# Kernel optimization log

Measured on AMD Instinct MI355X. Metric: run time of the kernel, lower is better.

The kernel has to match this reference:

```python
import jax, jax.numpy as jnp
import numpy as np

N, V, F, H, B, HID = 256, 32, 128, 8, 8, 64
R_MAX = 5.0
DH = F // H


def fc_edges(n):
    a = np.arange(n)
    s, r = np.meshgrid(a, a, indexing="ij")
    m = s != r
    return jnp.asarray(s[m]), jnp.asarray(r[m])

SENDERS, RECEIVERS = fc_edges(N)
E = N * (N - 1)


def sph_harmonics(u):
    # u: [..., 3] unit vectors -> [..., 15] = l=1(3)+l=2(5)+l=3(7), e3nn 'component' normalization
    x, y, z = u[..., 0], u[..., 1], u[..., 2]
    s3 = 3.0 ** 0.5; s5 = 5.0 ** 0.5; s7 = 7.0 ** 0.5
    s15 = 15.0 ** 0.5; s105 = 105.0 ** 0.5
    s35_8 = (35.0 / 8.0) ** 0.5; s21_8 = (21.0 / 8.0) ** 0.5
    l1 = [s3 * y, s3 * z, s3 * x]
    l2 = [s15 * x * y, s15 * y * z, 0.5 * s5 * (3 * z * z - 1),
          s15 * x * z, 0.5 * s15 * (x * x - y * y)]
    l3 = [s35_8 * y * (3 * x * x - y * y), s105 * x * y * z,
          s21_8 * y * (5 * z * z - 1), 0.5 * s7 * z * (5 * z * z - 3),
          s21_8 * x * (5 * z * z - 1), 0.5 * s105 * z * (x * x - y * y),
          s35_8 * x * (x * x - 3 * y * y)]
    return jnp.stack(l1 + l2 + l3, axis=-1)


def radial_embed(lengths):
    # Bessel basis (e3nn.bessel) times soft envelope (e3nn.soft_envelope)
    x = jnp.maximum(lengths, 1e-6)[..., None]
    k = jnp.arange(1, B + 1, dtype=lengths.dtype)
    bes = (2.0 / R_MAX) ** 0.5 * jnp.sin(k * jnp.pi * x / R_MAX) / x
    def sus(t):
        return jnp.where(t > 0, jnp.exp(-1.0 / jnp.where(t > 0, t, 1.0)), 0.0)
    env = 1.2 * sus(2.0 * (1.0 - lengths / R_MAX)) / sus(jnp.asarray(2.0))
    return bes * env[..., None]


def setup_inputs():
    key = jax.random.key(0)
    ks = jax.random.split(key, 16)
    def w(k, shape):
        return jax.random.normal(k, shape, jnp.float32) / (shape[0] ** 0.5)
    D_edge = 2 * F + V * B
    return {
        "positions": jax.random.normal(ks[0], (N, V, 3), jnp.float32),
        "features": jax.random.normal(ks[1], (N, F), jnp.float32),
        "We1": w(ks[2], (D_edge, HID)), "be1": jnp.zeros((HID,), jnp.float32),
        "We2": w(ks[3], (HID, HID)), "be2": jnp.zeros((HID,), jnp.float32),
        "W_q": w(ks[4], (F, F)), "W_k": w(ks[5], (HID, F)),
        "W_v": w(ks[6], (F, F)), "W_vec": w(ks[7], (HID, V)),
        "W_mix": w(ks[8], (V, V)),
        "M1": w(ks[9], (F, HID)), "bm1": jnp.zeros((HID,), jnp.float32),
        "M2": w(ks[10], (HID, HID)), "bm2": jnp.zeros((HID,), jnp.float32),
        "M3": w(ks[11], (HID, F)), "bm3": jnp.zeros((F,), jnp.float32),
    }


def reference(positions, features, We1, be1, We2, be2, W_q, W_k, W_v, W_vec,
              W_mix, M1, bm1, M2, bm2, M3, bm3):
    act = jax.nn.selu
    s, r = SENDERS, RECEIVERS
    vectors = positions[s] - positions[r]                        # [E, V, 3]
    lengths = jnp.sqrt(jnp.sum(vectors * vectors, -1) + 1e-18)   # [E, V] safe_norm
    unit = vectors / lengths[..., None]
    sph = sph_harmonics(unit)                                    # [E, V, 15]
    radial = radial_embed(lengths).reshape(E, V * B)             # [E, V*B]
    edge_weight_cutoff = jnp.ones((E,), positions.dtype)

    # edge MLP on invariants (radial embedding + src/dst scalar features)
    edge_in = jnp.concatenate([features[s], features[r], radial], -1)
    h = act(edge_in @ We1 + be1)
    h = act(h @ We2 + be2)                                       # [E, HID]

    # multi-head attention over incoming edges per node (segment softmax)
    q = (features @ W_q).reshape(N, H, DH)
    k = (h @ W_k).reshape(E, H, DH)
    logit = jnp.einsum("ehd,ehd->eh", k, q[r]) / (DH ** 0.5)
    lmax = jax.ops.segment_max(logit, r, num_segments=N)
    ex = edge_weight_cutoff[:, None] * jnp.exp(logit - lmax[r])
    denom = jax.ops.segment_sum(ex, r, num_segments=N)
    alpha = ex / (denom[r] + 1e-12)                              # [E, H]

    # invariant (0e) values
    v = (features[s] @ W_v).reshape(E, H, DH)
    inv_agg = jax.ops.segment_sum(alpha[..., None] * v, r, num_segments=N).reshape(N, F)

    # equivariant (1o) values: scalar-gated l=1 spherical harmonics (sqrt(3)*unit)
    coeff = h @ W_vec                                            # [E, V]
    alpha_v = jnp.repeat(alpha, V // H, axis=1)                  # [E, V]
    vec_msg = ((alpha_v * coeff) * (3.0 ** 0.5))[..., None] * unit  # [E, V, 3]
    vec_agg = jax.ops.segment_sum(vec_msg, r, num_segments=N)    # [N, V, 3]
    vec_out = jnp.einsum("nvc,vw->nwc", vec_agg, W_mix)

    # final invariant MLP + residuals
    hi = act(inv_agg @ M1 + bm1)
    hi = act(hi @ M2 + bm2)
    inv_out = hi @ M3 + bm3
    return (vec_out + positions, inv_out + features)
```

## Files before the change

kernel.cpp:

```cpp
#include <hip/hip_runtime.h>
#include <hip/hip_bf16.h>

#define NN 256
#define VC 32
#define FD 128

typedef unsigned int uint32;
typedef unsigned short u16;
typedef __attribute__((ext_vector_type(8))) short bf16x8;
typedef __attribute__((ext_vector_type(4))) float f32x4;

__device__ __forceinline__ float selu_f(float x) {
    const float lam = 1.0507009873554805f;
    const float la  = 1.7580993408473766f;
    return x > 0.f ? lam * x : la * (__expf(x) - 1.f);
}

__device__ __forceinline__ u16 f32_to_bf16_rne(float f) {
    uint32 u = __float_as_uint(f);
    uint32 r = (u + 0x7fffu + ((u >> 16) & 1u)) >> 16;
    return (u16)r;
}

__device__ __forceinline__ float bf16_to_f32(u16 h) {
    return __uint_as_float(((uint32)h) << 16);
}

__global__ __launch_bounds__(256) void k1_pre(
    const float* __restrict__ feat, const float* __restrict__ We1,
    const float* __restrict__ be1, const float* __restrict__ Wq,
    const float* __restrict__ Wk, const float* __restrict__ Wv,
    const float* __restrict__ Wvec, const float* __restrict__ We2,
    const float* __restrict__ pos,
    float* __restrict__ A, float* __restrict__ Bf, u16* __restrict__ kqb,
    u16* __restrict__ w1b, u16* __restrict__ we2b, u16* __restrict__ wvb,
    u16* __restrict__ fvtH, u16* __restrict__ fvtL,
    u16* __restrict__ ptH, u16* __restrict__ ptL,
    float* __restrict__ lgg2, u16* __restrict__ cfg2)
{
    __shared__ float fl[FD];
    __shared__ float ql[FD];
    const int n = blockIdx.x;
    const int t = threadIdx.x;
    {
        const int gid = n*256 + t;
        if (gid < 16384) {
            const int c = gid >> 8, k = gid & 255;
            w1b[gid] = f32_to_bf16_rne(We1[(256 + k)*64 + c]);
        } else if (gid < 20480) {
            const int o = gid - 16384;
            const int c = o >> 6, k = o & 63;
            we2b[o] = f32_to_bf16_rne(We2[k*64 + c]);
        } else if (gid < 22528) {
            const int o = gid - 20480;
            const int v = o >> 6, k = o & 63;
            wvb[o] = f32_to_bf16_rne(Wvec[k*32 + v]);
        }
    }
    if (t < FD) fl[t] = feat[n*FD + t];
    __syncthreads();
    if (t < 64) {
        float a = 0.f;
        for (int i = 0; i < FD; ++i) a = fmaf(fl[i], We1[i*64 + t], a);
        A[n*64 + t] = a;
    } else if (t < 128) {
        const int j = t - 64;
        float a = be1[j];
        for (int i = 0; i < FD; ++i) a = fmaf(fl[i], We1[(FD+i)*64 + j], a);
        Bf[n*64 + j] = a;
    } else {
        const int j = t - 128;
        float a = 0.f;
        for (int i = 0; i < FD; ++i) a = fmaf(fl[i], Wq[i*FD + j], a);
        ql[j] = a * 0.25f;
    }
    if (t < FD) {
        float a = 0.f;
        for (int i = 0; i < FD; ++i) a = fmaf(fl[i], Wv[i*FD + t], a);
        const u16 hi = f32_to_bf16_rne(a);
        const u16 lo = f32_to_bf16_rne(a - bf16_to_f32(hi));
        fvtH[t*256 + n] = hi;
        fvtL[t*256 + n] = lo;
    }
    if (t < 128) {
        const int v = t >> 2, c = t & 3;
        const float val = (c < 3) ? pos[(n*VC + v)*3 + c] : 1.0f;
        const u16 hi = f32_to_bf16_rne(val);
        const u16 lo = f32_to_bf16_rne(val - bf16_to_f32(hi));
        ptH[(v*4+c)*256 + n] = hi;
        ptL[(v*4+c)*256 + n] = lo;
    }
    if (t < 8)  lgg2[n*2048 + t*256 + n] = -1e30f;
    if (t < 32) cfg2[n*8192 + t*256 + n] = 0;
    __syncthreads();
    for (int o = t; o < 512; o += 256) {
        const int h = o >> 6, j = o & 63;
        float a = 0.f;
        #pragma unroll
        for (int d = 0; d < 16; ++d)
            a = fmaf(Wk[j*FD + h*16 + d], ql[h*16 + d], a);
        kqb[n*512 + o] = f32_to_bf16_rne(a);
    }
}

__global__ __launch_bounds__(256) void k2_edge(
    const float* __restrict__ pos, const float* __restrict__ be2,
    const float* __restrict__ Ag, const float* __restrict__ Bfg,
    const u16* __restrict__ w1b, const u16* __restrict__ we2b,
    const u16* __restrict__ wvb, const u16* __restrict__ kqb,
    float* __restrict__ lgg2, u16* __restrict__ cfg2)
{
    __shared__ u16 rad[8192];
    __shared__ u16 h1b[32*64];
    __shared__ u16 h2b[32*64];
    __shared__ float invl[32*33];

    const int t = threadIdx.x;
    const int wave = t >> 6, l = t & 63;
    const int li = l & 15, q = l >> 4;
    const int mh = wave >> 1, eh = wave & 1;
    const int r = blockIdx.x >> 2, part = blockIdx.x & 3;
    const int e = eh*16 + li;
    const int swz16 = (e & 7) << 3;

    bf16x8 w1A[2][8];
    #pragma unroll
    for (int mt = 0; mt < 2; ++mt) {
        const int c = mh*32 + mt*16 + li;
        #pragma unroll
        for (int kb = 0; kb < 8; ++kb)
            w1A[mt][kb] = *(const bf16x8*)(w1b + c*256 + kb*32 + q*8);
    }
    bf16x8 we2A[2][2];
    #pragma unroll
    for (int mt = 0; mt < 2; ++mt) {
        const int c2 = mh*32 + mt*16 + li;
        #pragma unroll
        for (int kb = 0; kb < 2; ++kb)
            we2A[mt][kb] = *(const bf16x8*)(we2b + c2*64 + kb*32 + q*8);
    }
    bf16x8 wvA[2];
    {
        const int v = mh*16 + li;
        #pragma unroll
        for (int kb = 0; kb < 2; ++kb)
            wvA[kb] = *(const bf16x8*)(wvb + v*64 + kb*32 + q*8);
    }
    bf16x8 kqA[2];
    if (li < 8) {
        #pragma unroll
        for (int kb = 0; kb < 2; ++kb)
            kqA[kb] = *(const bf16x8*)(kqb + r*512 + li*64 + kb*32 + q*8);
    } else {
        #pragma unroll
        for (int kb = 0; kb < 2; ++kb)
            #pragma unroll
            for (int j = 0; j < 8; ++j) kqA[kb][j] = 0;
    }
    float bfreg[2][4], be2reg[2][4];
    #pragma unroll
    for (int mt = 0; mt < 2; ++mt)
        #pragma unroll
        for (int rg = 0; rg < 4; ++rg) {
            const int c = mh*32 + mt*16 + q*4 + rg;
            bfreg[mt][rg] = Bfg[r*64 + c];
            be2reg[mt][rg] = be2[c];
        }

    for (int it = 0; it < 2; ++it) {
        const int s0 = (part*2 + it) * 32;
        const int sp = s0 + e;
        int s = sp + (sp >= r ? 1 : 0); if (s > 255) s = 255;
        __syncthreads();

        float As[2][4];
        #pragma unroll
        for (int mt = 0; mt < 2; ++mt)
            #pragma unroll
            for (int rg = 0; rg < 4; ++rg)
                As[mt][rg] = Ag[s*64 + mh*32 + mt*16 + q*4 + rg];

        {
            const int ep = t & 31, vg = t >> 5;
            const int spp = s0 + ep;
            int sv = spp + (spp >= r ? 1 : 0); if (sv > 255) sv = 255;
            #pragma unroll
            for (int kk = 0; kk < 4; ++kk) {
                const int v = vg*4 + kk;
                const float* ps = pos + (sv*VC + v)*3;
                const float* pr = pos + (r*VC + v)*3;
                const float dx = ps[0]-pr[0], dy = ps[1]-pr[1], dz = ps[2]-pr[2];
                const float d2 = fmaf(dx,dx,fmaf(dy,dy,dz*dz)) + 1e-18f;
                const float len = sqrtf(d2);
                invl[ep*33 + v] = rsqrtf(d2);
                const float x = fmaxf(len, 1e-6f);
                const float tt2 = 2.f - 0.4f*len;
                const float env = tt2 > 0.f ? 1.9784655248401538f * __expf(-1.f/tt2) : 0.f;
                const float coefc = 0.6324555320336759f * env / x;
                float s_cur, c1;
                __sincosf(0.6283185307179586f * x, &s_cur, &c1);
                const float c2x = 2.f * c1;
                float s_prev = 0.f;
                union { uint4 u4; u16 us[8]; } pk;
                #pragma unroll
                for (int b = 0; b < 8; ++b) {
                    pk.us[b] = f32_to_bf16_rne(coefc * s_cur);
                    const float s_next = fmaf(c2x, s_cur, -s_prev);
                    s_prev = s_cur; s_cur = s_next;
                }
                *(uint4*)((char*)rad + ((ep*512 + v*16) ^ ((ep & 15) << 4))) = pk.u4;
            }
        }
        __syncthreads();

        f32x4 d1[2] = {{0.f,0.f,0.f,0.f},{0.f,0.f,0.f,0.f}};
        #pragma unroll
        for (int kb = 0; kb < 8; ++kb) {
            const bf16x8 rf = *(const bf16x8*)((const char*)rad +
                                ((e*512 + (kb*4+q)*16) ^ ((e & 15) << 4)));
            d1[0] = __builtin_amdgcn_mfma_f32_16x16x32_bf16(w1A[0][kb], rf, d1[0], 0, 0, 0);
            d1[1] = __builtin_amdgcn_mfma_f32_16x16x32_bf16(w1A[1][kb], rf, d1[1], 0, 0, 0);
        }
        #pragma unroll
        for (int mt = 0; mt < 2; ++mt) {
            const int c0 = mh*32 + mt*16 + q*4;
            const u16 p0 = f32_to_bf16_rne(selu_f(d1[mt][0] + As[mt][0] + bfreg[mt][0]));
            const u16 p1 = f32_to_bf16_rne(selu_f(d1[mt][1] + As[mt][1] + bfreg[mt][1]));
            const u16 p2 = f32_to_bf16_rne(selu_f(d1[mt][2] + As[mt][2] + bfreg[mt][2]));
            const u16 p3 = f32_to_bf16_rne(selu_f(d1[mt][3] + As[mt][3] + bfreg[mt][3]));
            *(uint32*)&h1b[e*64 + ((c0)     ^ swz16)] = (uint32)p0 | ((uint32)p1 << 16);
            *(uint32*)&h1b[e*64 + ((c0 + 2) ^ swz16)] = (uint32)p2 | ((uint32)p3 << 16);
        }
        __syncthreads();

        f32x4 d2[2] = {{0.f,0.f,0.f,0.f},{0.f,0.f,0.f,0.f}};
        #pragma unroll
        for (int kb = 0; kb < 2; ++kb) {
            const bf16x8 hb = *(const bf16x8*)&h1b[e*64 + ((kb*32 + q*8) ^ swz16)];
            d2[0] = __builtin_amdgcn_mfma_f32_16x16x32_bf16(we2A[0][kb], hb, d2[0], 0, 0, 0);
            d2[1] = __builtin_amdgcn_mfma_f32_16x16x32_bf16(we2A[1][kb], hb, d2[1], 0, 0, 0);
        }
        #pragma unroll
        for (int mt = 0; mt < 2; ++mt) {
            const int c0 = mh*32 + mt*16 + q*4;
            const u16 p0 = f32_to_bf16_rne(selu_f(d2[mt][0] + be2reg[mt][0]));
            const u16 p1 = f32_to_bf16_rne(selu_f(d2[mt][1] + be2reg[mt][1]));
            const u16 p2 = f32_to_bf16_rne(selu_f(d2[mt][2] + be2reg[mt][2]));
            const u16 p3 = f32_to_bf16_rne(selu_f(d2[mt][3] + be2reg[mt][3]));
            *(uint32*)&h2b[e*64 + ((c0)     ^ swz16)] = (uint32)p0 | ((uint32)p1 << 16);
            *(uint32*)&h2b[e*64 + ((c0 + 2) ^ swz16)] = (uint32)p2 | ((uint32)p3 << 16);
        }
        __syncthreads();

        f32x4 d3 = {0.f,0.f,0.f,0.f};
        f32x4 dl = {0.f,0.f,0.f,0.f};
        #pragma unroll
        for (int kb = 0; kb < 2; ++kb) {
            const bf16x8 hb = *(const bf16x8*)&h2b[e*64 + ((kb*32 + q*8) ^ swz16)];
            d3 = __builtin_amdgcn_mfma_f32_16x16x32_bf16(wvA[kb], hb, d3, 0, 0, 0);
            if (mh == 0)
                dl = __builtin_amdgcn_mfma_f32_16x16x32_bf16(kqA[kb], hb, dl, 0, 0, 0);
        }
        if (sp < 255) {
            #pragma unroll
            for (int rg = 0; rg < 4; ++rg) {
                const int v = mh*16 + q*4 + rg;
                cfg2[(size_t)r*8192 + v*256 + s] =
                    f32_to_bf16_rne(d3[rg] * 1.7320508075688772f * invl[e*33 + v]);
            }
            if (mh == 0 && q < 2) {
                #pragma unroll
                for (int rg = 0; rg < 4; ++rg)
                    lgg2[(size_t)r*2048 + (q*4+rg)*256 + s] = dl[rg];
            }
        }
    }
}

__global__ __launch_bounds__(64) void k3b_agg(
    const float* __restrict__ lgg2, const u16* __restrict__ cfg2,
    const u16* __restrict__ fvtH, const u16* __restrict__ fvtL,
    const u16* __restrict__ ptH, const u16* __restrict__ ptL,
    float* __restrict__ inv, float* __restrict__ vec4)
{
    const int l = threadIdx.x, li = l & 15, q = l >> 4;
    const int b = blockIdx.x;
    if (b < 128) {
        const int h = b >> 4, r0 = (b & 15) * 16;
        bf16x8 fH[8], fL[8];
        #pragma unroll
        for (int kb = 0; kb < 8; ++kb) {
            fH[kb] = *(const bf16x8*)(fvtH + (h*16+li)*256 + kb*32 + q*8);
            fL[kb] = *(const bf16x8*)(fvtL + (h*16+li)*256 + kb*32 + q*8);
        }
        const float* lgr = lgg2 + (size_t)(r0+li)*2048 + h*256;
        float mx = -3.0e38f;
        #pragma unroll
        for (int kb = 0; kb < 8; ++kb) {
            const float4 g0 = *(const float4*)(lgr + kb*32 + q*8);
            const float4 g1 = *(const float4*)(lgr + kb*32 + q*8 + 4);
            mx = fmaxf(mx, fmaxf(fmaxf(g0.x,g0.y), fmaxf(g0.z,g0.w)));
            mx = fmaxf(mx, fmaxf(fmaxf(g1.x,g1.y), fmaxf(g1.z,g1.w)));
        }
        mx = fmaxf(mx, __shfl_xor(mx, 16));
        mx = fmaxf(mx, __shfl_xor(mx, 32));
        float sm = 0.f;
        f32x4 Ch = {0.f,0.f,0.f,0.f};
        f32x4 Cl = {0.f,0.f,0.f,0.f};
        #pragma unroll
        for (int kb = 0; kb < 8; ++kb) {
            const float4 g0 = *(const float4*)(lgr + kb*32 + q*8);
            const float4 g1 = *(const float4*)(lgr + kb*32 + q*8 + 4);
            float ev[8];
            ev[0]=__expf(g0.x-mx); ev[1]=__expf(g0.y-mx); ev[2]=__expf(g0.z-mx); ev[3]=__expf(g0.w-mx);
            ev[4]=__expf(g1.x-mx); ev[5]=__expf(g1.y-mx); ev[6]=__expf(g1.z-mx); ev[7]=__expf(g1.w-mx);
            bf16x8 a;
            #pragma unroll
            for (int j = 0; j < 8; ++j) { sm += ev[j]; a[j] = (short)f32_to_bf16_rne(ev[j]); }
            Ch = __builtin_amdgcn_mfma_f32_16x16x32_bf16(a, fH[kb], Ch, 0, 0, 0);
            Cl = __builtin_amdgcn_mfma_f32_16x16x32_bf16(a, fL[kb], Cl, 0, 0, 0);
        }
        sm += __shfl_xor(sm, 16);
        sm += __shfl_xor(sm, 32);
        #pragma unroll
        for (int rg = 0; rg < 4; ++rg) {
            const float d = __shfl(sm, q*4 + rg);
            inv[(r0 + q*4 + rg)*128 + h*16 + li] = (Ch[rg] + Cl[rg]) / (d + 1e-12f);
        }
    } else {
        const int b2 = b - 128, v = b2 >> 4, r0 = (b2 & 15) * 16;
        const int h = v >> 2;
        bf16x8 pH[8], pL[8];
        #pragma unroll
        for (int kb = 0; kb < 8; ++kb) {
            if (li < 4) {
                pH[kb] = *(const bf16x8*)(ptH + (v*4+li)*256 + kb*32 + q*8);
                pL[kb] = *(const bf16x8*)(ptL + (v*4+li)*256 + kb*32 + q*8);
            } else {
                #pragma unroll
                for (int j = 0; j < 8; ++j) { pH[kb][j] = 0; pL[kb][j] = 0; }
            }
        }
        const float* lgr = lgg2 + (size_t)(r0+li)*2048 + h*256;
        const u16*  cfr = cfg2 + (size_t)(r0+li)*8192 + v*256;
        float mx = -3.0e38f;
        #pragma unroll
        for (int kb = 0; kb < 8; ++kb) {
            const float4 g0 = *(const float4*)(lgr + kb*32 + q*8);
            const float4 g1 = *(const float4*)(lgr + kb*32 + q*8 + 4);
            mx = fmaxf(mx, fmaxf(fmaxf(g0.x,g0.y), fmaxf(g0.z,g0.w)));
            mx = fmaxf(mx, fmaxf(fmaxf(g1.x,g1.y), fmaxf(g1.z,g1.w)));
        }
        mx = fmaxf(mx, __shfl_xor(mx, 16));
        mx = fmaxf(mx, __shfl_xor(mx, 32));
        float sm = 0.f;
        f32x4 Ch = {0.f,0.f,0.f,0.f};
        f32x4 Cl = {0.f,0.f,0.f,0.f};
        #pragma unroll
        for (int kb = 0; kb < 8; ++kb) {
            const float4 g0 = *(const float4*)(lgr + kb*32 + q*8);
            const float4 g1 = *(const float4*)(lgr + kb*32 + q*8 + 4);
            const bf16x8 cf8 = *(const bf16x8*)(cfr + kb*32 + q*8);
            float ev[8];
            ev[0]=__expf(g0.x-mx); ev[1]=__expf(g0.y-mx); ev[2]=__expf(g0.z-mx); ev[3]=__expf(g0.w-mx);
            ev[4]=__expf(g1.x-mx); ev[5]=__expf(g1.y-mx); ev[6]=__expf(g1.z-mx); ev[7]=__expf(g1.w-mx);
            bf16x8 a;
            #pragma unroll
            for (int j = 0; j < 8; ++j) {
                sm += ev[j];
                a[j] = (short)f32_to_bf16_rne(ev[j] * bf16_to_f32((u16)cf8[j]));
            }
            Ch = __builtin_amdgcn_mfma_f32_16x16x32_bf16(a, pH[kb], Ch, 0, 0, 0);
            Cl = __builtin_amdgcn_mfma_f32_16x16x32_bf16(a, pL[kb], Cl, 0, 0, 0);
        }
        sm += __shfl_xor(sm, 16);
        sm += __shfl_xor(sm, 32);
        #pragma unroll
        for (int rg = 0; rg < 4; ++rg) {
            const float d = __shfl(sm, q*4 + rg);
            if (li < 4)
                vec4[(r0 + q*4 + rg)*128 + v*4 + li] = (Ch[rg] + Cl[rg]) / (d + 1e-12f);
        }
    }
}

__global__ __launch_bounds__(64) void k3c_out(
    const float* __restrict__ pos, const float* __restrict__ feat,
    const float* __restrict__ inv, const float* __restrict__ vec4,
    const float* __restrict__ Wmix,
    const float* __restrict__ M1, const float* __restrict__ bm1,
    const float* __restrict__ M2, const float* __restrict__ bm2,
    const float* __restrict__ M3, const float* __restrict__ bm3,
    float* __restrict__ out0, float* __restrict__ out1)
{
    __shared__ float inva[128];
    __shared__ float vec4s[128];
    __shared__ float pos96[96];
    __shared__ float vecl[96];
    __shared__ float hi1[64];
    __shared__ float hi2[64];
    const int r = blockIdx.x;
    const int l = threadIdx.x;
    inva[l]       = inv[r*128 + l];
    inva[64 + l]  = inv[r*128 + 64 + l];
    vec4s[l]      = vec4[r*128 + l];
    vec4s[64 + l] = vec4[r*128 + 64 + l];
    for (int o = l; o < 96; o += 64) pos96[o] = pos[r*96 + o];
    __syncthreads();
    for (int o = l; o < 96; o += 64) {
        const int v = o / 3, c = o - v*3;
        vecl[o] = vec4s[v*4 + c] - vec4s[v*4 + 3] * pos96[o];
    }
    float a1 = bm1[l];
    #pragma unroll 8
    for (int k = 0; k < 128; ++k) a1 = fmaf(inva[k], M1[k*64 + l], a1);
    hi1[l] = selu_f(a1);
    __syncthreads();
    float a2 = bm2[l];
    #pragma unroll 8
    for (int k = 0; k < 64; ++k) a2 = fmaf(hi1[k], M2[k*64 + l], a2);
    hi2[l] = selu_f(a2);
    __syncthreads();
    #pragma unroll
    for (int o0 = 0; o0 < 128; o0 += 64) {
        const int o = o0 + l;
        float a = bm3[o];
        #pragma unroll 8
        for (int k = 0; k < 64; ++k) a = fmaf(hi2[k], M3[k*128 + o], a);
        out1[r*128 + o] = a + feat[r*128 + o];
    }
    for (int o = l; o < 96; o += 64) {
        const int w = o / 3, c = o - w*3;
        float a = 0.f;
        #pragma unroll
        for (int v = 0; v < 32; ++v)
            a = fmaf(vecl[v*3 + c], Wmix[v*32 + w], a);
        out0[r*96 + o] = a + pos96[o];
    }
}

extern "C" void kernel_launch(void* const* d_in, const int* in_sizes, int n_in,
                              void* d_out, int out_size, void* d_ws, size_t ws_size,
                              hipStream_t stream)
{
    const float* pos  = (const float*)d_in[0];
    const float* feat = (const float*)d_in[1];
    const float* We1  = (const float*)d_in[2];
    const float* be1  = (const float*)d_in[3];
    const float* We2  = (const float*)d_in[4];
    const float* be2  = (const float*)d_in[5];
    const float* Wq   = (const float*)d_in[6];
    const float* Wk   = (const float*)d_in[7];
    const float* Wv   = (const float*)d_in[8];
    const float* Wvec = (const float*)d_in[9];
    const float* Wmix = (const float*)d_in[10];
    const float* M1   = (const float*)d_in[11];
    const float* bm1  = (const float*)d_in[12];
    const float* M2   = (const float*)d_in[13];
    const float* bm2  = (const float*)d_in[14];
    const float* M3   = (const float*)d_in[15];
    const float* bm3  = (const float*)d_in[16];

    char* ws = (char*)d_ws;
    float* A    = (float*)(ws + 0);
    float* Bf   = (float*)(ws + 65536);
    u16*   kqb  = (u16*)(ws + 131072);
    u16*   w1b  = (u16*)(ws + 393216);
    u16*   we2b = (u16*)(ws + 425984);
    u16*   wvb  = (u16*)(ws + 434176);
    u16*   fvtH = (u16*)(ws + 438272);
    u16*   fvtL = (u16*)(ws + 503808);
    u16*   ptH  = (u16*)(ws + 569344);
    u16*   ptL  = (u16*)(ws + 634880);
    float* lgg2 = (float*)(ws + 700416);
    u16*   cfg2 = (u16*)(ws + 2797568);
    float* inv   = (float*)(ws + 0);
    float* vec4  = (float*)(ws + 131072);
    if (ws_size < (size_t)6991872) return;

    float* out0 = (float*)d_out;
    float* out1 = out0 + NN*VC*3;

    hipLaunchKernelGGL(k1_pre, dim3(256), dim3(256), 0, stream,
                       feat, We1, be1, Wq, Wk, Wv, Wvec, We2, pos,
                       A, Bf, kqb, w1b, we2b, wvb, fvtH, fvtL, ptH, ptL, lgg2, cfg2);
    hipLaunchKernelGGL(k2_edge, dim3(1024), dim3(256), 0, stream,
                       pos, be2, A, Bf, w1b, we2b, wvb, kqb, lgg2, cfg2);
    hipLaunchKernelGGL(k3b_agg, dim3(640), dim3(64), 0, stream,
                       lgg2, cfg2, fvtH, fvtL, ptH, ptL, inv, vec4);
    hipLaunchKernelGGL(k3c_out, dim3(256), dim3(64), 0, stream,
                       pos, feat, inv, vec4, Wmix,
                       M1, bm1, M2, bm2, M3, bm3, out0, out1);
}
```

Measured before the change: 53.73 us.

## Fuse pipeline into one cooperative persistent kernel with grid syncs

Merges the precompute, edge MLP, and aggregation stages into a single cooperative kernel that uses grid-wide syncs instead of separate launches. Work is redistributed across blocks: the Wv and position transposes move to a second set of virtual blocks, and each edge block now handles four chunks of 32 senders. The output kernel is widened to 256 threads with a split-K partial sum for the first MLP layer. The intent is to remove inter-kernel launch gaps and tail idle time. The cost is grid-sync overhead, the occupancy limits a cooperative launch imposes, and larger register and shared-memory pressure from the union layout. A fallback path relaunches separate kernels if the cooperative launch fails.

```diff
diff --git a/kernel.cpp b/kernel.cpp
--- a/kernel.cpp
+++ b/kernel.cpp
@@ -1,5 +1,8 @@
 #include <hip/hip_runtime.h>
 #include <hip/hip_bf16.h>
+#include <hip/hip_cooperative_groups.h>
+
+namespace cg = cooperative_groups;
 
 #define NN 256
 #define VC 32
@@ -26,100 +29,450 @@
     return __uint_as_float(((uint32)h) << 16);
 }
 
-__global__ __launch_bounds__(256) void k1_pre(
-    const float* __restrict__ feat, const float* __restrict__ We1,
-    const float* __restrict__ be1, const float* __restrict__ Wq,
-    const float* __restrict__ Wk, const float* __restrict__ Wv,
-    const float* __restrict__ Wvec, const float* __restrict__ We2,
-    const float* __restrict__ pos,
-    float* __restrict__ A, float* __restrict__ Bf, u16* __restrict__ kqb,
-    u16* __restrict__ w1b, u16* __restrict__ we2b, u16* __restrict__ wvb,
-    u16* __restrict__ fvtH, u16* __restrict__ fvtL,
-    u16* __restrict__ ptH, u16* __restrict__ ptL,
-    float* __restrict__ lgg2, u16* __restrict__ cfg2)
+struct Params {
+    const float *pos, *feat, *We1, *be1, *We2, *be2, *Wq, *Wk, *Wv, *Wvec,
+                *Wmix, *M1, *bm1, *M2, *bm2, *M3, *bm3;
+    float *A, *Bf;
+    u16 *kqb, *w1b, *we2b, *wvb, *fvtH, *fvtL, *ptH, *ptL;
+    float *lgg2;
+    u16 *cfg2;
+    float *inv, *vec4;
+    float *out0, *out1;
+};
+
+__device__ __forceinline__ void phase1_node(const Params& P, int vb, int t,
+                                            float* fl, float* ql)
+{
+    if (vb < 256) {
+        const int n = vb;
+        {
+            const int gid = n*256 + t;
+            if (gid < 16384) {
+                const int c = gid >> 8, k = gid & 255;
+                P.w1b[gid] = f32_to_bf16_rne(P.We1[(256 + k)*64 + c]);
+            } else if (gid < 20480) {
+                const int o = gid - 16384;
+                const int c = o >> 6, k = o & 63;
+                P.we2b[o] = f32_to_bf16_rne(P.We2[k*64 + c]);
+            } else if (gid < 22528) {
+                const int o = gid - 20480;
+                const int v = o >> 6, k = o & 63;
+                P.wvb[o] = f32_to_bf16_rne(P.Wvec[k*32 + v]);
+            }
+        }
+        if (t < FD) fl[t] = P.feat[n*FD + t];
+        __syncthreads();
+        if (t < 64) {
+            float a = 0.f;
+            for (int i = 0; i < FD; ++i) a = fmaf(fl[i], P.We1[i*64 + t], a);
+            P.A[n*64 + t] = a;
+        } else if (t < 128) {
+            const int j = t - 64;
+            float a = P.be1[j];
+            for (int i = 0; i < FD; ++i) a = fmaf(fl[i], P.We1[(FD+i)*64 + j], a);
+            P.Bf[n*64 + j] = a;
+        } else {
+            const int j = t - 128;
+            float a = 0.f;
+            for (int i = 0; i < FD; ++i) a = fmaf(fl[i], P.Wq[i*FD + j], a);
+            ql[j] = a * 0.25f;
+        }
+        if (t < 8)  P.lgg2[n*2048 + t*256 + n] = -1e30f;
+        if (t < 32) P.cfg2[(size_t)n*8192 + t*256 + n] = 0;
+        __syncthreads();
+        for (int o = t; o < 512; o += 256) {
+            const int h = o >> 6, j = o & 63;
+            float a = 0.f;
+            #pragma unroll
+            for (int d = 0; d < 16; ++d)
+                a = fmaf(P.Wk[j*FD + h*16 + d], ql[h*16 + d], a);
+            P.kqb[n*512 + o] = f32_to_bf16_rne(a);
+        }
+    } else {
+        const int n = vb - 256;
+        if (t < FD) fl[t] = P.feat[n*FD + t];
+        __syncthreads();
+        if (t < FD) {
+            float a = 0.f;
+            for (int i = 0; i < FD; ++i) a = fmaf(fl[i], P.Wv[i*FD + t], a);
+            const u16 hi = f32_to_bf16_rne(a);
+            const u16 lo = f32_to_bf16_rne(a - bf16_to_f32(hi));
+            P.fvtH[t*256 + n] = hi;
+            P.fvtL[t*256 + n] = lo;
+            const int v = t >> 2, c = t & 3;
+            const float val = (c < 3) ? P.pos[(n*VC + v)*3 + c] : 1.0f;
+            const u16 phi = f32_to_bf16_rne(val);
+            const u16 plo = f32_to_bf16_rne(val - bf16_to_f32(phi));
+            P.ptH[(v*4+c)*256 + n] = phi;
+            P.ptL[(v*4+c)*256 + n] = plo;
+        }
+    }
+}
+
+__global__ __launch_bounds__(256, 2) void mega(Params P)
+{
+    __shared__ union {
+        struct { float fl[128]; float ql[128]; } p1;
+        struct { u16 rad[8192]; u16 h1b[2048]; u16 h2b[2048]; float invl[1056]; } p2;
+        struct { float part[4][64]; float inva[128]; float vec4s[128];
+                 float pos96[96]; float vecl[96]; float hi1[64]; float hi2[64]; } p4;
+    } smem;
+    cg::grid_group grid = cg::this_grid();
+    const int b = blockIdx.x;
+    const int nbx = gridDim.x;
+    const int t = threadIdx.x;
+
+    for (int vb = b; vb < 512; vb += nbx) {
+        __syncthreads();
+        phase1_node(P, vb, t, smem.p1.fl, smem.p1.ql);
+    }
+    grid.sync();
+
+    {
+        const int wave = t >> 6, l = t & 63;
+        const int li = l & 15, q = l >> 4;
+        const int mh = wave >> 1, eh = wave & 1;
+        const int e = eh*16 + li;
+        const int swz16 = (e & 7) << 3;
+
+        bf16x8 w1A[2][8];
+        #pragma unroll
+        for (int mt = 0; mt < 2; ++mt) {
+            const int c = mh*32 + mt*16 + li;
+            #pragma unroll
+            for (int kb = 0; kb < 8; ++kb)
+                w1A[mt][kb] = *(const bf16x8*)(P.w1b + c*256 + kb*32 + q*8);
+        }
+        bf16x8 we2A[2][2];
+        #pragma unroll
+        for (int mt = 0; mt < 2; ++mt) {
+            const int c2 = mh*32 + mt*16 + li;
+            #pragma unroll
+            for (int kb = 0; kb < 2; ++kb)
+                we2A[mt][kb] = *(const bf16x8*)(P.we2b + c2*64 + kb*32 + q*8);
+        }
+        bf16x8 wvA[2];
+        {
+            const int v = mh*16 + li;
+            #pragma unroll
+            for (int kb = 0; kb < 2; ++kb)
+                wvA[kb] = *(const bf16x8*)(P.wvb + v*64 + kb*32 + q*8);
+        }
+        float be2reg[2][4];
+        #pragma unroll
+        for (int mt = 0; mt < 2; ++mt)
+            #pragma unroll
+            for (int rg = 0; rg < 4; ++rg)
+                be2reg[mt][rg] = P.be2[mh*32 + mt*16 + q*4 + rg];
+
+        for (int vb = b; vb < 512; vb += nbx) {
+            const int r = vb >> 1, tpart = vb & 1;
+            bf16x8 kqA[2];
+            if (li < 8) {
+                #pragma unroll
+                for (int kb = 0; kb < 2; ++kb)
+                    kqA[kb] = *(const bf16x8*)(P.kqb + r*512 + li*64 + kb*32 + q*8);
+            } else {
+                #pragma unroll
+                for (int kb = 0; kb < 2; ++kb)
+                    #pragma unroll
+                    for (int j = 0; j < 8; ++j) kqA[kb][j] = 0;
+            }
+            float bfreg[2][4];
+            #pragma unroll
+            for (int mt = 0; mt < 2; ++mt)
+                #pragma unroll
+                for (int rg = 0; rg < 4; ++rg)
+                    bfreg[mt][rg] = P.Bf[r*64 + mh*32 + mt*16 + q*4 + rg];
+
+            for (int it = 0; it < 4; ++it) {
+                const int s0 = (tpart*4 + it) * 32;
+                const int sp = s0 + e;
+                int s = sp + (sp >= r ? 1 : 0); if (s > 255) s = 255;
+                __syncthreads();
+
+                float As[2][4];
+                #pragma unroll
+                for (int mt = 0; mt < 2; ++mt)
+                    #pragma unroll
+                    for (int rg = 0; rg < 4; ++rg)
+                        As[mt][rg] = P.A[s*64 + mh*32 + mt*16 + q*4 + rg];
+
+                {
+                    const int ep = t & 31, vg = t >> 5;
+                    const int spp = s0 + ep;
+                    int sv = spp + (spp >= r ? 1 : 0); if (sv > 255) sv = 255;
+                    #pragma unroll
+                    for (int kk = 0; kk < 4; ++kk) {
+                        const int v = vg*4 + kk;
+                        const float* ps = P.pos + (sv*VC + v)*3;
+                        const float* pr = P.pos + (r*VC + v)*3;
+                        const float dx = ps[0]-pr[0], dy = ps[1]-pr[1], dz = ps[2]-pr[2];
+                        const float d2 = fmaf(dx,dx,fmaf(dy,dy,dz*dz)) + 1e-18f;
+                        const float len = sqrtf(d2);
+                        smem.p2.invl[ep*33 + v] = rsqrtf(d2);
+                        const float x = fmaxf(len, 1e-6f);
+                        const float tt2 = 2.f - 0.4f*len;
+                        const float env = tt2 > 0.f ? 1.9784655248401538f * __expf(-1.f/tt2) : 0.f;
+                        const float coefc = 0.6324555320336759f * env / x;
+                        float s_cur, c1;
+                        __sincosf(0.6283185307179586f * x, &s_cur, &c1);
+                        const float c2x = 2.f * c1;
+                        float s_prev = 0.f;
+                        union { uint4 u4; u16 us[8]; } pk;
+                        #pragma unroll
+                        for (int bb = 0; bb < 8; ++bb) {
+                            pk.us[bb] = f32_to_bf16_rne(coefc * s_cur);
+                            const float s_next = fmaf(c2x, s_cur, -s_prev);
+                            s_prev = s_cur; s_cur = s_next;
+                        }
+                        *(uint4*)((char*)smem.p2.rad + ((ep*512 + v*16) ^ ((ep & 15) << 4))) = pk.u4;
+                    }
+                }
+                __syncthreads();
+
+                f32x4 d1[2] = {{0.f,0.f,0.f,0.f},{0.f,0.f,0.f,0.f}};
+                #pragma unroll
+                for (int kb = 0; kb < 8; ++kb) {
+                    const bf16x8 rf = *(const bf16x8*)((const char*)smem.p2.rad +
+                                        ((e*512 + (kb*4+q)*16) ^ ((e & 15) << 4)));
+                    d1[0] = __builtin_amdgcn_mfma_f32_16x16x32_bf16(w1A[0][kb], rf, d1[0], 0, 0, 0);
+                    d1[1] = __builtin_amdgcn_mfma_f32_16x16x32_bf16(w1A[1][kb], rf, d1[1], 0, 0, 0);
+                }
+                #pragma unroll
+                for (int mt = 0; mt < 2; ++mt) {
+                    const int c0 = mh*32 + mt*16 + q*4;
+                    const u16 p0 = f32_to_bf16_rne(selu_f(d1[mt][0] + As[mt][0] + bfreg[mt][0]));
+                    const u16 p1 = f32_to_bf16_rne(selu_f(d1[mt][1] + As[mt][1] + bfreg[mt][1]));
+                    const u16 p2 = f32_to_bf16_rne(selu_f(d1[mt][2] + As[mt][2] + bfreg[mt][2]));
+                    const u16 p3 = f32_to_bf16_rne(selu_f(d1[mt][3] + As[mt][3] + bfreg[mt][3]));
+                    *(uint32*)&smem.p2.h1b[e*64 + ((c0)     ^ swz16)] = (uint32)p0 | ((uint32)p1 << 16);
+                    *(uint32*)&smem.p2.h1b[e*64 + ((c0 + 2) ^ swz16)] = (uint32)p2 | ((uint32)p3 << 16);
+                }
+                __syncthreads();
+
+                f32x4 d2[2] = {{0.f,0.f,0.f,0.f},{0.f,0.f,0.f,0.f}};
+                #pragma unroll
+                for (int kb = 0; kb < 2; ++kb) {
+                    const bf16x8 hb = *(const bf16x8*)&smem.p2.h1b[e*64 + ((kb*32 + q*8) ^ swz16)];
+                    d2[0] = __builtin_amdgcn_mfma_f32_16x16x32_bf16(we2A[0][kb], hb, d2[0], 0, 0, 0);
+                    d2[1] = __builtin_amdgcn_mfma_f32_16x16x32_bf16(we2A[1][kb], hb, d2[1], 0, 0, 0);
+                }
+                #pragma unroll
+                for (int mt = 0; mt < 2; ++mt) {
+                    const int c0 = mh*32 + mt*16 + q*4;
+                    const u16 p0 = f32_to_bf16_rne(selu_f(d2[mt][0] + be2reg[mt][0]));
+                    const u16 p1 = f32_to_bf16_rne(selu_f(d2[mt][1] + be2reg[mt][1]));
+                    const u16 p2 = f32_to_bf16_rne(selu_f(d2[mt][2] + be2reg[mt][2]));
+                    const u16 p3 = f32_to_bf16_rne(selu_f(d2[mt][3] + be2reg[mt][3]));
+                    *(uint32*)&smem.p2.h2b[e*64 + ((c0)     ^ swz16)] = (uint32)p0 | ((uint32)p1 << 16);
+                    *(uint32*)&smem.p2.h2b[e*64 + ((c0 + 2) ^ swz16)] = (uint32)p2 | ((uint32)p3 << 16);
+                }
+                __syncthreads();
+
+                f32x4 d3 = {0.f,0.f,0.f,0.f};
+                f32x4 dl = {0.f,0.f,0.f,0.f};
+                #pragma unroll
+                for (int kb = 0; kb < 2; ++kb) {
+                    const bf16x8 hb = *(const bf16x8*)&smem.p2.h2b[e*64 + ((kb*32 + q*8) ^ swz16)];
+                    d3 = __builtin_amdgcn_mfma_f32_16x16x32_bf16(wvA[kb], hb, d3, 0, 0, 0);
+                    if (mh == 0)
+                        dl = __builtin_amdgcn_mfma_f32_16x16x32_bf16(kqA[kb], hb, dl, 0, 0, 0);
+                }
+                if (sp < 255) {
+                    #pragma unroll
+                    for (int rg = 0; rg < 4; ++rg) {
+                        const int v = mh*16 + q*4 + rg;
+                        P.cfg2[(size_t)r*8192 + v*256 + s] =
+                            f32_to_bf16_rne(d3[rg] * 1.7320508075688772f * smem.p2.invl[e*33 + v]);
+                    }
+                    if (mh == 0 && q < 2) {
+                        #pragma unroll
+                        for (int rg = 0; rg < 4; ++rg)
+                            P.lgg2[(size_t)r*2048 + (q*4+rg)*256 + s] = dl[rg];
+                    }
+                }
+            }
+        }
+    }
+    grid.sync();
+
+    {
+        const int wv = t >> 6, l = t & 63;
+        const int li = l & 15, q = l >> 4;
+        for (int task = wv*nbx + b; task < 640; task += 4*nbx) {
+            if (task < 128) {
+                const int h = task >> 4, r0 = (task & 15) * 16;
+                bf16x8 fH[8], fL[8];
+                #pragma unroll
+                for (int kb = 0; kb < 8; ++kb) {
+                    fH[kb] = *(const bf16x8*)(P.fvtH + (h*16+li)*256 + kb*32 + q*8);
+                    fL[kb] = *(const bf16x8*)(P.fvtL + (h*16+li)*256 + kb*32 + q*8);
+                }
+                const float* lgr = P.lgg2 + (size_t)(r0+li)*2048 + h*256;
+                float mx = -3.0e38f;
+                #pragma unroll
+                for (int kb = 0; kb < 8; ++kb) {
+                    const float4 g0 = *(const float4*)(lgr + kb*32 + q*8);
+                    const float4 g1 = *(const float4*)(lgr + kb*32 + q*8 + 4);
+                    mx = fmaxf(mx, fmaxf(fmaxf(g0.x,g0.y), fmaxf(g0.z,g0.w)));
+                    mx = fmaxf(mx, fmaxf(fmaxf(g1.x,g1.y), fmaxf(g1.z,g1.w)));
+                }
+                mx = fmaxf(mx, __shfl_xor(mx, 16));
+                mx = fmaxf(mx, __shfl_xor(mx, 32));
+                float ssum = 0.f;
+                f32x4 Ch = {0.f,0.f,0.f,0.f};
+                f32x4 Cl = {0.f,0.f,0.f,0.f};
+                #pragma unroll
+                for (int kb = 0; kb < 8; ++kb) {
+                    const float4 g0 = *(const float4*)(lgr + kb*32 + q*8);
+                    const float4 g1 = *(const float4*)(lgr + kb*32 + q*8 + 4);
+                    float ev[8];
+                    ev[0]=__expf(g0.x-mx); ev[1]=__expf(g0.y-mx); ev[2]=__expf(g0.z-mx); ev[3]=__expf(g0.w-mx);
+                    ev[4]=__expf(g1.x-mx); ev[5]=__expf(g1.y-mx); ev[6]=__expf(g1.z-mx); ev[7]=__expf(g1.w-mx);
+                    bf16x8 a;
+                    #pragma unroll
+                    for (int j = 0; j < 8; ++j) { ssum += ev[j]; a[j] = (short)f32_to_bf16_rne(ev[j]); }
+                    Ch = __builtin_amdgcn_mfma_f32_16x16x32_bf16(a, fH[kb], Ch, 0, 0, 0);
+                    Cl = __builtin_amdgcn_mfma_f32_16x16x32_bf16(a, fL[kb], Cl, 0, 0, 0);
+                }
+                ssum += __shfl_xor(ssum, 16);
+                ssum += __shfl_xor(ssum, 32);
+                #pragma unroll
+                for (int rg = 0; rg < 4; ++rg) {
+                    const float d = __shfl(ssum, q*4 + rg);
+                    P.inv[(r0 + q*4 + rg)*128 + h*16 + li] = (Ch[rg] + Cl[rg]) / (d + 1e-12f);
+                }
+            } else {
+                const int b2 = task - 128, v = b2 >> 4, r0 = (b2 & 15) * 16;
+                const int h = v >> 2;
+                bf16x8 pH[8], pL[8];
+                #pragma unroll
+                for (int kb = 0; kb < 8; ++kb) {
+                    if (li < 4) {
+                        pH[kb] = *(const bf16x8*)(P.ptH + (v*4+li)*256 + kb*32 + q*8);
+                        pL[kb] = *(const bf16x8*)(P.ptL + (v*4+li)*256 + kb*32 + q*8);
+                    } else {
+                        #pragma unroll
+                        for (int j = 0; j < 8; ++j) { pH[kb][j] = 0; pL[kb][j] = 0; }
+                    }
+                }
+                const float* lgr = P.lgg2 + (size_t)(r0+li)*2048 + h*256;
+                const u16*  cfr = P.cfg2 + (size_t)(r0+li)*8192 + v*256;
+                float mx = -3.0e38f;
+                #pragma unroll
+                for (int kb = 0; kb < 8; ++kb) {
+                    const float4 g0 = *(const float4*)(lgr + kb*32 + q*8);
+                    const float4 g1 = *(const float4*)(lgr + kb*32 + q*8 + 4);
+                    mx = fmaxf(mx, fmaxf(fmaxf(g0.x,g0.y), fmaxf(g0.z,g0.w)));
+                    mx = fmaxf(mx, fmaxf(fmaxf(g1.x,g1.y), fmaxf(g1.z,g1.w)));
+                }
+                mx = fmaxf(mx, __shfl_xor(mx, 16));
+                mx = fmaxf(mx, __shfl_xor(mx, 32));
+                float ssum = 0.f;
+                f32x4 Ch = {0.f,0.f,0.f,0.f};
+                f32x4 Cl = {0.f,0.f,0.f,0.f};
+                #pragma unroll
+                for (int kb = 0; kb < 8; ++kb) {
+                    const float4 g0 = *(const float4*)(lgr + kb*32 + q*8);
+                    const float4 g1 = *(const float4*)(lgr + kb*32 + q*8 + 4);
+                    const bf16x8 cf8 = *(const bf16x8*)(cfr + kb*32 + q*8);
+                    float ev[8];
+                    ev[0]=__expf(g0.x-mx); ev[1]=__expf(g0.y-mx); ev[2]=__expf(g0.z-mx); ev[3]=__expf(g0.w-mx);
+                    ev[4]=__expf(g1.x-mx); ev[5]=__expf(g1.y-mx); ev[6]=__expf(g1.z-mx); ev[7]=__expf(g1.w-mx);
+                    bf16x8 a;
+                    #pragma unroll
+                    for (int j = 0; j < 8; ++j) {
+                        ssum += ev[j];
+                        a[j] = (short)f32_to_bf16_rne(ev[j] * bf16_to_f32((u16)cf8[j]));
+                    }
+                    Ch = __builtin_amdgcn_mfma_f32_16x16x32_bf16(a, pH[kb], Ch, 0, 0, 0);
+                    Cl = __builtin_amdgcn_mfma_f32_16x16x32_bf16(a, pL[kb], Cl, 0, 0, 0);
+                }
+                ssum += __shfl_xor(ssum, 16);
+                ssum += __shfl_xor(ssum, 32);
+                #pragma unroll
+                for (int rg = 0; rg < 4; ++rg) {
+                    const float d = __shfl(ssum, q*4 + rg);
+                    if (li < 4)
+                        P.vec4[(r0 + q*4 + rg)*128 + v*4 + li] = (Ch[rg] + Cl[rg]) / (d + 1e-12f);
+                }
+            }
+        }
+    }
+    grid.sync();
+
+    for (int r = b; r < 256; r += nbx) {
+        __syncthreads();
+        if (t < 128) smem.p4.inva[t] = P.inv[r*128 + t];
+        else         smem.p4.vec4s[t-128] = P.vec4[r*128 + (t-128)];
+        if (t < 96)  smem.p4.pos96[t] = P.pos[r*96 + t];
+        __syncthreads();
+        if (t < 96) {
+            const int v = t / 3, c = t - v*3;
+            smem.p4.vecl[t] = smem.p4.vec4s[v*4 + c] - smem.p4.vec4s[v*4 + 3] * smem.p4.pos96[t];
+        }
+        {
+            const int f = t & 63, g = t >> 6;
+            const int k0 = g*32;
+            float acc = 0.f;
+            #pragma unroll 8
+            for (int k = k0; k < k0 + 32; ++k)
+                acc = fmaf(smem.p4.inva[k], P.M1[k*64 + f], acc);
+            smem.p4.part[g][f] = acc;
+        }
+        __syncthreads();
+        if (t < 64) {
+            const float a1 = P.bm1[t] + smem.p4.part[0][t] + smem.p4.part[1][t]
+                           + smem.p4.part[2][t] + smem.p4.part[3][t];
+            smem.p4.hi1[t] = selu_f(a1);
+        }
+        __syncthreads();
+        if (t < 64) {
+            float a2 = P.bm2[t];
+            #pragma unroll 8
+            for (int k = 0; k < 64; ++k) a2 = fmaf(smem.p4.hi1[k], P.M2[k*64 + t], a2);
+            smem.p4.hi2[t] = selu_f(a2);
+        }
+        __syncthreads();
+        if (t < 128) {
+            float a = P.bm3[t];
+            #pragma unroll 8
+            for (int k = 0; k < 64; ++k) a = fmaf(smem.p4.hi2[k], P.M3[k*128 + t], a);
+            P.out1[r*128 + t] = a + P.feat[r*128 + t];
+        } else if (t < 224) {
+            const int o = t - 128;
+            const int w = o / 3, c = o - w*3;
+            float a = 0.f;
+            #pragma unroll
+            for (int v = 0; v < 32; ++v)
+                a = fmaf(smem.p4.vecl[v*3 + c], P.Wmix[v*32 + w], a);
+            P.out0[r*96 + o] = a + smem.p4.pos96[o];
+        }
+    }
+}
+
+__global__ __launch_bounds__(256) void k1_pre(Params P)
 {
     __shared__ float fl[FD];
     __shared__ float ql[FD];
-    const int n = blockIdx.x;
-    const int t = threadIdx.x;
-    {
-        const int gid = n*256 + t;
-        if (gid < 16384) {
-            const int c = gid >> 8, k = gid & 255;
-            w1b[gid] = f32_to_bf16_rne(We1[(256 + k)*64 + c]);
-        } else if (gid < 20480) {
-            const int o = gid - 16384;
-            const int c = o >> 6, k = o & 63;
-            we2b[o] = f32_to_bf16_rne(We2[k*64 + c]);
-        } else if (gid < 22528) {
-            const int o = gid - 20480;
-            const int v = o >> 6, k = o & 63;
-            wvb[o] = f32_to_bf16_rne(Wvec[k*32 + v]);
-        }
-    }
-    if (t < FD) fl[t] = feat[n*FD + t];
+    phase1_node(P, blockIdx.x, threadIdx.x, fl, ql);
     __syncthreads();
-    if (t < 64) {
-        float a = 0.f;
-        for (int i = 0; i < FD; ++i) a = fmaf(fl[i], We1[i*64 + t], a);
-        A[n*64 + t] = a;
-    } else if (t < 128) {
-        const int j = t - 64;
-        float a = be1[j];
-        for (int i = 0; i < FD; ++i) a = fmaf(fl[i], We1[(FD+i)*64 + j], a);
-        Bf[n*64 + j] = a;
-    } else {
-        const int j = t - 128;
-        float a = 0.f;
-        for (int i = 0; i < FD; ++i) a = fmaf(fl[i], Wq[i*FD + j], a);
-        ql[j] = a * 0.25f;
-    }
-    if (t < FD) {
-        float a = 0.f;
-        for (int i = 0; i < FD; ++i) a = fmaf(fl[i], Wv[i*FD + t], a);
-        const u16 hi = f32_to_bf16_rne(a);
-        const u16 lo = f32_to_bf16_rne(a - bf16_to_f32(hi));
-        fvtH[t*256 + n] = hi;
-        fvtL[t*256 + n] = lo;
-    }
-    if (t < 128) {
-        const int v = t >> 2, c = t & 3;
-        const float val = (c < 3) ? pos[(n*VC + v)*3 + c] : 1.0f;
-        const u16 hi = f32_to_bf16_rne(val);
-        const u16 lo = f32_to_bf16_rne(val - bf16_to_f32(hi));
-        ptH[(v*4+c)*256 + n] = hi;
-        ptL[(v*4+c)*256 + n] = lo;
-    }
-    if (t < 8)  lgg2[n*2048 + t*256 + n] = -1e30f;
-    if (t < 32) cfg2[n*8192 + t*256 + n] = 0;
-    __syncthreads();
-    for (int o = t; o < 512; o += 256) {
-        const int h = o >> 6, j = o & 63;
-        float a = 0.f;
-        #pragma unroll
-        for (int d = 0; d < 16; ++d)
-            a = fmaf(Wk[j*FD + h*16 + d], ql[h*16 + d], a);
-        kqb[n*512 + o] = f32_to_bf16_rne(a);
-    }
-}
-
-__global__ __launch_bounds__(256) void k2_edge(
-    const float* __restrict__ pos, const float* __restrict__ be2,
-    const float* __restrict__ Ag, const float* __restrict__ Bfg,
-    const u16* __restrict__ w1b, const u16* __restrict__ we2b,
-    const u16* __restrict__ wvb, const u16* __restrict__ kqb,
-    float* __restrict__ lgg2, u16* __restrict__ cfg2)
+    phase1_node(P, blockIdx.x + 256, threadIdx.x, fl, ql);
+}
+
+__global__ __launch_bounds__(256) void k2_edge(Params P)
 {
     __shared__ u16 rad[8192];
-    __shared__ u16 h1b[32*64];
-    __shared__ u16 h2b[32*64];
-    __shared__ float invl[32*33];
+    __shared__ u16 h1b[2048];
+    __shared__ u16 h2b[2048];
+    __shared__ float invl[1056];
 
     const int t = threadIdx.x;
     const int wave = t >> 6, l = t & 63;
     const int li = l & 15, q = l >> 4;
     const int mh = wave >> 1, eh = wave & 1;
-    const int r = blockIdx.x >> 2, part = blockIdx.x & 3;
+    const int r = blockIdx.x >> 1, tpart = blockIdx.x & 1;
     const int e = eh*16 + li;
     const int swz16 = (e & 7) << 3;
 
@@ -129,7 +482,7 @@
         const int c = mh*32 + mt*16 + li;
         #pragma unroll
         for (int kb = 0; kb < 8; ++kb)
-            w1A[mt][kb] = *(const bf16x8*)(w1b + c*256 + kb*32 + q*8);
+            w1A[mt][kb] = *(const bf16x8*)(P.w1b + c*256 + kb*32 + q*8);
     }
     bf16x8 we2A[2][2];
     #pragma unroll
@@ -137,20 +490,20 @@
         const int c2 = mh*32 + mt*16 + li;
         #pragma unroll
         for (int kb = 0; kb < 2; ++kb)
-            we2A[mt][kb] = *(const bf16x8*)(we2b + c2*64 + kb*32 + q*8);
+            we2A[mt][kb] = *(const bf16x8*)(P.we2b + c2*64 + kb*32 + q*8);
     }
     bf16x8 wvA[2];
     {
         const int v = mh*16 + li;
         #pragma unroll
         for (int kb = 0; kb < 2; ++kb)
-            wvA[kb] = *(const bf16x8*)(wvb + v*64 + kb*32 + q*8);
+            wvA[kb] = *(const bf16x8*)(P.wvb + v*64 + kb*32 + q*8);
     }
     bf16x8 kqA[2];
     if (li < 8) {
         #pragma unroll
         for (int kb = 0; kb < 2; ++kb)
-            kqA[kb] = *(const bf16x8*)(kqb + r*512 + li*64 + kb*32 + q*8);
+            kqA[kb] = *(const bf16x8*)(P.kqb + r*512 + li*64 + kb*32 + q*8);
     } else {
         #pragma unroll
         for (int kb = 0; kb < 2; ++kb)
@@ -163,12 +516,12 @@
         #pragma unroll
         for (int rg = 0; rg < 4; ++rg) {
             const int c = mh*32 + mt*16 + q*4 + rg;
-            bfreg[mt][rg] = Bfg[r*64 + c];
-            be2reg[mt][rg] = be2[c];
-        }
-
-    for (int it = 0; it < 2; ++it) {
-        const int s0 = (part*2 + it) * 32;
+            bfreg[mt][rg] = P.Bf[r*64 + c];
+            be2reg[mt][rg] = P.be2[c];
+        }
+
+    for (int it = 0; it < 4; ++it) {
+        const int s0 = (tpart*4 + it) * 32;
         const int sp = s0 + e;
         int s = sp + (sp >= r ? 1 : 0); if (s > 255) s = 255;
         __syncthreads();
@@ -178,7 +531,7 @@
         for (int mt = 0; mt < 2; ++mt)
             #pragma unroll
             for (int rg = 0; rg < 4; ++rg)
-                As[mt][rg] = Ag[s*64 + mh*32 + mt*16 + q*4 + rg];
+                As[mt][rg] = P.A[s*64 + mh*32 + mt*16 + q*4 + rg];
 
         {
             const int ep = t & 31, vg = t >> 5;
@@ -187,8 +540,8 @@
             #pragma unroll
             for (int kk = 0; kk < 4; ++kk) {
                 const int v = vg*4 + kk;
-                const float* ps = pos + (sv*VC + v)*3;
-                const float* pr = pos + (r*VC + v)*3;
+                const float* ps = P.pos + (sv*VC + v)*3;
+                const float* pr = P.pos + (r*VC + v)*3;
                 const float dx = ps[0]-pr[0], dy = ps[1]-pr[1], dz = ps[2]-pr[2];
                 const float d2 = fmaf(dx,dx,fmaf(dy,dy,dz*dz)) + 1e-18f;
                 const float len = sqrtf(d2);
@@ -203,8 +556,8 @@
                 float s_prev = 0.f;
                 union { uint4 u4; u16 us[8]; } pk;
                 #pragma unroll
-                for (int b = 0; b < 8; ++b) {
-                    pk.us[b] = f32_to_bf16_rne(coefc * s_cur);
+                for (int bb = 0; bb < 8; ++bb) {
+                    pk.us[bb] = f32_to_bf16_rne(coefc * s_cur);
                     const float s_next = fmaf(c2x, s_cur, -s_prev);
                     s_prev = s_cur; s_cur = s_next;
                 }
@@ -265,35 +618,31 @@
             #pragma unroll
             for (int rg = 0; rg < 4; ++rg) {
                 const int v = mh*16 + q*4 + rg;
-                cfg2[(size_t)r*8192 + v*256 + s] =
+                P.cfg2[(size_t)r*8192 + v*256 + s] =
                     f32_to_bf16_rne(d3[rg] * 1.7320508075688772f * invl[e*33 + v]);
             }
             if (mh == 0 && q < 2) {
                 #pragma unroll
                 for (int rg = 0; rg < 4; ++rg)
-                    lgg2[(size_t)r*2048 + (q*4+rg)*256 + s] = dl[rg];
+                    P.lgg2[(size_t)r*2048 + (q*4+rg)*256 + s] = dl[rg];
             }
         }
     }
 }
 
-__global__ __launch_bounds__(64) void k3b_agg(
-    const float* __restrict__ lgg2, const u16* __restrict__ cfg2,
-    const u16* __restrict__ fvtH, const u16* __restrict__ fvtL,
-    const u16* __restrict__ ptH, const u16* __restrict__ ptL,
-    float* __restrict__ inv, float* __restrict__ vec4)
+__global__ __launch_bounds__(64) void k3b_agg(Params P)
 {
     const int l = threadIdx.x, li = l & 15, q = l >> 4;
-    const int b = blockIdx.x;
-    if (b < 128) {
-        const int h = b >> 4, r0 = (b & 15) * 16;
+    const int task = blockIdx.x;
+    if (task < 128) {
+        const int h = task >> 4, r0 = (task & 15) * 16;
         bf16x8 fH[8], fL[8];
         #pragma unroll
         for (int kb = 0; kb < 8; ++kb) {
-            fH[kb] = *(const bf16x8*)(fvtH + (h*16+li)*256 + kb*32 + q*8);
-            fL[kb] = *(const bf16x8*)(fvtL + (h*16+li)*256 + kb*32 + q*8);
-        }
-        const float* lgr = lgg2 + (size_t)(r0+li)*2048 + h*256;
+            fH[kb] = *(const bf16x8*)(P.fvtH + (h*16+li)*256 + kb*32 + q*8);
+            fL[kb] = *(const bf16x8*)(P.fvtL + (h*16+li)*256 + kb*32 + q*8);
+        }
+        const float* lgr = P.lgg2 + (size_t)(r0+li)*2048 + h*256;
         float mx = -3.0e38f;
         #pragma unroll
         for (int kb = 0; kb < 8; ++kb) {
@@ -304,7 +653,7 @@
         }
         mx = fmaxf(mx, __shfl_xor(mx, 16));
         mx = fmaxf(mx, __shfl_xor(mx, 32));
-        float sm = 0.f;
+        float ssum = 0.f;
         f32x4 Ch = {0.f,0.f,0.f,0.f};
         f32x4 Cl = {0.f,0.f,0.f,0.f};
         #pragma unroll
@@ -316,33 +665,33 @@
             ev[4]=__expf(g1.x-mx); ev[5]=__expf(g1.y-mx); ev[6]=__expf(g1.z-mx); ev[7]=__expf(g1.w-mx);
             bf16x8 a;
             #pragma unroll
-            for (int j = 0; j < 8; ++j) { sm += ev[j]; a[j] = (short)f32_to_bf16_rne(ev[j]); }
+            for (int j = 0; j < 8; ++j) { ssum += ev[j]; a[j] = (short)f32_to_bf16_rne(ev[j]); }
             Ch = __builtin_amdgcn_mfma_f32_16x16x32_bf16(a, fH[kb], Ch, 0, 0, 0);
             Cl = __builtin_amdgcn_mfma_f32_16x16x32_bf16(a, fL[kb], Cl, 0, 0, 0);
         }
-        sm += __shfl_xor(sm, 16);
-        sm += __shfl_xor(sm, 32);
+        ssum += __shfl_xor(ssum, 16);
+        ssum += __shfl_xor(ssum, 32);
         #pragma unroll
         for (int rg = 0; rg < 4; ++rg) {
-            const float d = __shfl(sm, q*4 + rg);
-            inv[(r0 + q*4 + rg)*128 + h*16 + li] = (Ch[rg] + Cl[rg]) / (d + 1e-12f);
+            const float d = __shfl(ssum, q*4 + rg);
+            P.inv[(r0 + q*4 + rg)*128 + h*16 + li] = (Ch[rg] + Cl[rg]) / (d + 1e-12f);
         }
     } else {
-        const int b2 = b - 128, v = b2 >> 4, r0 = (b2 & 15) * 16;
+        const int b2 = task - 128, v = b2 >> 4, r0 = (b2 & 15) * 16;
         const int h = v >> 2;
         bf16x8 pH[8], pL[8];
         #pragma unroll
         for (int kb = 0; kb < 8; ++kb) {
             if (li < 4) {
-                pH[kb] = *(const bf16x8*)(ptH + (v*4+li)*256 + kb*32 + q*8);
-                pL[kb] = *(const bf16x8*)(ptL + (v*4+li)*256 + kb*32 + q*8);
+                pH[kb] = *(const bf16x8*)(P.ptH + (v*4+li)*256 + kb*32 + q*8);
+                pL[kb] = *(const bf16x8*)(P.ptL + (v*4+li)*256 + kb*32 + q*8);
             } else {
                 #pragma unroll
                 for (int j = 0; j < 8; ++j) { pH[kb][j] = 0; pL[kb][j] = 0; }
             }
         }
-        const float* lgr = lgg2 + (size_t)(r0+li)*2048 + h*256;
-        const u16*  cfr = cfg2 + (size_t)(r0+li)*8192 + v*256;
+        const float* lgr = P.lgg2 + (size_t)(r0+li)*2048 + h*256;
+        const u16*  cfr = P.cfg2 + (size_t)(r0+li)*8192 + v*256;
         float mx = -3.0e38f;
         #pragma unroll
         for (int kb = 0; kb < 8; ++kb) {
@@ -353,7 +702,7 @@
         }
         mx = fmaxf(mx, __shfl_xor(mx, 16));
         mx = fmaxf(mx, __shfl_xor(mx, 32));
-        float sm = 0.f;
+        float ssum = 0.f;
         f32x4 Ch = {0.f,0.f,0.f,0.f};
         f32x4 Cl = {0.f,0.f,0.f,0.f};
         #pragma unroll
@@ -367,32 +716,26 @@
             bf16x8 a;
             #pragma unroll
             for (int j = 0; j < 8; ++j) {
-                sm += ev[j];
+                ssum += ev[j];
                 a[j] = (short)f32_to_bf16_rne(ev[j] * bf16_to_f32((u16)cf8[j]));
             }
             Ch = __builtin_amdgcn_mfma_f32_16x16x32_bf16(a, pH[kb], Ch, 0, 0, 0);
             Cl = __builtin_amdgcn_mfma_f32_16x16x32_bf16(a, pL[kb], Cl, 0, 0, 0);
         }
-        sm += __shfl_xor(sm, 16);
-        sm += __shfl_xor(sm, 32);
+        ssum += __shfl_xor(ssum, 16);
+        ssum += __shfl_xor(ssum, 32);
         #pragma unroll
         for (int rg = 0; rg < 4; ++rg) {
-            const float d = __shfl(sm, q*4 + rg);
+            const float d = __shfl(ssum, q*4 + rg);
             if (li < 4)
-                vec4[(r0 + q*4 + rg)*128 + v*4 + li] = (Ch[rg] + Cl[rg]) / (d + 1e-12f);
-        }
-    }
-}
-
-__global__ __launch_bounds__(64) void k3c_out(
-    const float* __restrict__ pos, const float* __restrict__ feat,
-    const float* __restrict__ inv, const float* __restrict__ vec4,
-    const float* __restrict__ Wmix,
-    const float* __restrict__ M1, const float* __restrict__ bm1,
-    const float* __restrict__ M2, const float* __restrict__ bm2,
-    const float* __restrict__ M3, const float* __restrict__ bm3,
-    float* __restrict__ out0, float* __restrict__ out1)
+                P.vec4[(r0 + q*4 + rg)*128 + v*4 + li] = (Ch[rg] + Cl[rg]) / (d + 1e-12f);
+        }
+    }
+}
+
+__global__ __launch_bounds__(256) void k3c_out(Params P)
 {
+    __shared__ float part[4][64];
     __shared__ float inva[128];
     __shared__ float vec4s[128];
     __shared__ float pos96[96];
@@ -400,42 +743,50 @@
     __shared__ float hi1[64];
     __shared__ float hi2[64];
     const int r = blockIdx.x;
-    const int l = threadIdx.x;
-    inva[l]       = inv[r*128 + l];
-    inva[64 + l]  = inv[r*128 + 64 + l];
-    vec4s[l]      = vec4[r*128 + l];
-    vec4s[64 + l] = vec4[r*128 + 64 + l];
-    for (int o = l; o < 96; o += 64) pos96[o] = pos[r*96 + o];
+    const int t = threadIdx.x;
+    if (t < 128) inva[t] = P.inv[r*128 + t];
+    else         vec4s[t-128] = P.vec4[r*128 + (t-128)];
+    if (t < 96)  pos96[t] = P.pos[r*96 + t];
     __syncthreads();
-    for (int o = l; o < 96; o += 64) {
-        const int v = o / 3, c = o - v*3;
-        vecl[o] = vec4s[v*4 + c] - vec4s[v*4 + 3] * pos96[o];
-    }
-    float a1 = bm1[l];
-    #pragma unroll 8
-    for (int k = 0; k < 128; ++k) a1 = fmaf(inva[k], M1[k*64 + l], a1);
-    hi1[l] = selu_f(a1);
+    if (t < 96) {
+        const int v = t / 3, c = t - v*3;
+        vecl[t] = vec4s[v*4 + c] - vec4s[v*4 + 3] * pos96[t];
+    }
+    {
+        const int f = t & 63, g = t >> 6;
+        const int k0 = g*32;
+        float acc = 0.f;
+        #pragma unroll 8
+        for (int k = k0; k < k0 + 32; ++k)
+            acc = fmaf(inva[k], P.M1[k*64 + f], acc);
+        part[g][f] = acc;
+    }
     __syncthreads();
-    float a2 = bm2[l];
-    #pragma unroll 8
-    for (int k = 0; k < 64; ++k) a2 = fmaf(hi1[k], M2[k*64 + l], a2);
-    hi2[l] = selu_f(a2);
+    if (t < 64) {
+        const float a1 = P.bm1[t] + part[0][t] + part[1][t] + part[2][t] + part[3][t];
+        hi1[t] = selu_f(a1);
+    }
     __syncthreads();
-    #pragma unroll
-    for (int o0 = 0; o0 < 128; o0 += 64) {
-        const int o = o0 + l;
-        float a = bm3[o];
+    if (t < 64) {
+        float a2 = P.bm2[t];
         #pragma unroll 8
-        for (int k = 0; k < 64; ++k) a = fmaf(hi2[k], M3[k*128 + o], a);
-        out1[r*128 + o] = a + feat[r*128 + o];
-    }
-    for (int o = l; o < 96; o += 64) {
+        for (int k = 0; k < 64; ++k) a2 = fmaf(hi1[k], P.M2[k*64 + t], a2);
+        hi2[t] = selu_f(a2);
+    }
+    __syncthreads();
+    if (t < 128) {
+        float a = P.bm3[t];
+        #pragma unroll 8
+        for (int k = 0; k < 64; ++k) a = fmaf(hi2[k], P.M3[k*128 + t], a);
+        P.out1[r*128 + t] = a + P.feat[r*128 + t];
+    } else if (t < 224) {
+        const int o = t - 128;
         const int w = o / 3, c = o - w*3;
         float a = 0.f;
         #pragma unroll
         for (int v = 0; v < 32; ++v)
-            a = fmaf(vecl[v*3 + c], Wmix[v*32 + w], a);
-        out0[r*96 + o] = a + pos96[o];
+            a = fmaf(vecl[v*3 + c], P.Wmix[v*32 + w], a);
+        P.out0[r*96 + o] = a + pos96[o];
     }
 }
 
@@ -443,52 +794,60 @@
                               void* d_out, int out_size, void* d_ws, size_t ws_size,
                               hipStream_t stream)
 {
-    const float* pos  = (const float*)d_in[0];
-    const float* feat = (const float*)d_in[1];
-    const float* We1  = (const float*)d_in[2];
-    const float* be1  = (const float*)d_in[3];
-    const float* We2  = (const float*)d_in[4];
-    const float* be2  = (const float*)d_in[5];
-    const float* Wq   = (const float*)d_in[6];
-    const float* Wk   = (const float*)d_in[7];
-    const float* Wv   = (const float*)d_in[8];
-    const float* Wvec = (const float*)d_in[9];
-    const float* Wmix = (const float*)d_in[10];
-    const float* M1   = (const float*)d_in[11];
-    const float* bm1  = (const float*)d_in[12];
-    const float* M2   = (const float*)d_in[13];
-    const float* bm2  = (const float*)d_in[14];
-    const float* M3   = (const float*)d_in[15];
-    const float* bm3  = (const float*)d_in[16];
-
     char* ws = (char*)d_ws;
-    float* A    = (float*)(ws + 0);
-    float* Bf   = (float*)(ws + 65536);
-    u16*   kqb  = (u16*)(ws + 131072);
-    u16*   w1b  = (u16*)(ws + 393216);
-    u16*   we2b = (u16*)(ws + 425984);
-    u16*   wvb  = (u16*)(ws + 434176);
-    u16*   fvtH = (u16*)(ws + 438272);
-    u16*   fvtL = (u16*)(ws + 503808);
-    u16*   ptH  = (u16*)(ws + 569344);
-    u16*   ptL  = (u16*)(ws + 634880);
-    float* lgg2 = (float*)(ws + 700416);
-    u16*   cfg2 = (u16*)(ws + 2797568);
-    float* inv   = (float*)(ws + 0);
-    float* vec4  = (float*)(ws + 131072);
     if (ws_size < (size_t)6991872) return;
 
-    float* out0 = (float*)d_out;
-    float* out1 = out0 + NN*VC*3;
-
-    hipLaunchKernelGGL(k1_pre, dim3(256), dim3(256), 0, stream,
-                       feat, We1, be1, Wq, Wk, Wv, Wvec, We2, pos,
-                       A, Bf, kqb, w1b, we2b, wvb, fvtH, fvtL, ptH, ptL, lgg2, cfg2);
-    hipLaunchKernelGGL(k2_edge, dim3(1024), dim3(256), 0, stream,
-                       pos, be2, A, Bf, w1b, we2b, wvb, kqb, lgg2, cfg2);
-    hipLaunchKernelGGL(k3b_agg, dim3(640), dim3(64), 0, stream,
-                       lgg2, cfg2, fvtH, fvtL, ptH, ptL, inv, vec4);
-    hipLaunchKernelGGL(k3c_out, dim3(256), dim3(64), 0, stream,
-                       pos, feat, inv, vec4, Wmix,
-                       M1, bm1, M2, bm2, M3, bm3, out0, out1);
-}
+    Params p;
+    p.pos  = (const float*)d_in[0];
+    p.feat = (const float*)d_in[1];
+    p.We1  = (const float*)d_in[2];
+    p.be1  = (const float*)d_in[3];
+    p.We2  = (const float*)d_in[4];
+    p.be2  = (const float*)d_in[5];
+    p.Wq   = (const float*)d_in[6];
+    p.Wk   = (const float*)d_in[7];
+    p.Wv   = (const float*)d_in[8];
+    p.Wvec = (const float*)d_in[9];
+    p.Wmix = (const float*)d_in[10];
+    p.M1   = (const float*)d_in[11];
+    p.bm1  = (const float*)d_in[12];
+    p.M2   = (const float*)d_in[13];
+    p.bm2  = (const float*)d_in[14];
+    p.M3   = (const float*)d_in[15];
+    p.bm3  = (const float*)d_in[16];
+
+    p.A    = (float*)(ws + 0);
+    p.Bf   = (float*)(ws + 65536);
+    p.kqb  = (u16*)(ws + 131072);
+    p.w1b  = (u16*)(ws + 393216);
+    p.we2b = (u16*)(ws + 425984);
+    p.wvb  = (u16*)(ws + 434176);
+    p.fvtH = (u16*)(ws + 438272);
+    p.fvtL = (u16*)(ws + 503808);
+    p.ptH  = (u16*)(ws + 569344);
+    p.ptL  = (u16*)(ws + 634880);
+    p.lgg2 = (float*)(ws + 700416);
+    p.cfg2 = (u16*)(ws + 2797568);
+    p.inv  = (float*)(ws + 0);
+    p.vec4 = (float*)(ws + 131072);
+
+    p.out0 = (float*)d_out;
+    p.out1 = p.out0 + NN*VC*3;
+
+    bool done = false;
+    int occ = 0;
+    if (hipOccupancyMaxActiveBlocksPerMultiprocessor(&occ, (const void*)mega, 256, 0)
+            == hipSuccess && occ >= 1) {
+        const int nb = (occ >= 2) ? 512 : 256;
+        void* args[] = { (void*)&p };
+        if (hipLaunchCooperativeKernel((const void*)mega, dim3(nb), dim3(256),
+                                       args, 0, stream) == hipSuccess)
+            done = true;
+    }
+    if (!done) {
+        hipLaunchKernelGGL(k1_pre,  dim3(256),  dim3(256), 0, stream, p);
+        hipLaunchKernelGGL(k2_edge, dim3(512),  dim3(256), 0, stream, p);
+        hipLaunchKernelGGL(k3b_agg, dim3(640),  dim3(64),  0, stream, p);
+        hipLaunchKernelGGL(k3c_out, dim3(256),  dim3(256), 0, stream, p);
+    }
+}
```

Result: slower. 161.9 us (+201.3%).
